# Kernel optimization log

Hardware: AMD Instinct MI355X
Metric: run time of the kernel (lower is better)

The kernel has to match this reference:

```python
import jax, jax.numpy as jnp
import numpy as np

B, T, D, H = 8, 512, 1024, 16
DH = D // H
MAX_LEN = 512  # max_pos_encoding


def rel_pos_encoding(seq_len, dim):
    # Relative sinusoidal PE, full (non-causal) context, no hidden state.
    # positions: max_len-1 ... 1, 0, -1 ... -(max_len-1)
    pos = jnp.concatenate([
        jnp.arange(MAX_LEN - 1, 0, -1, dtype=jnp.float32),
        jnp.arange(0, -MAX_LEN, -1, dtype=jnp.float32),
    ])  # (2*max_len-1,)
    inv_freq = jnp.power(10000.0, -2.0 * jnp.arange(dim // 2, dtype=jnp.float32) / dim)
    ang = pos[:, None] * inv_freq[None, :]  # (2M-1, D/2)
    pe = jnp.zeros((2 * MAX_LEN - 1, dim), dtype=jnp.float32)
    pe = pe.at[:, 0::2].set(jnp.sin(ang)).at[:, 1::2].set(jnp.cos(ang))
    # non-causal slice: [max_len - seq_len : max_len - 1 + seq_len] -> 2T-1 rows
    return pe[MAX_LEN - seq_len: MAX_LEN - 1 + seq_len]


def rel_to_abs(s):
    # full-context skewing (Bello et al.): s is (B, H, T1, T2) with T2 = 2*T1 - 1
    b, h, t1, t2 = s.shape
    s = jnp.pad(s, ((0, 0), (0, 0), (0, 0), (0, 1)))
    s = s.reshape(b, h, t1 * (t2 + 1))
    s = jnp.pad(s, ((0, 0), (0, 0), (0, t2 - t1)))
    s = s.reshape(b, h, t1 + 1, t2)
    return s[:, :, :t1, t1 - 1:]  # (B, H, T1, T1)


def setup_inputs() -> dict:
    key = jax.random.key(0)
    ks = jax.random.split(key, 9)
    sc = 1.0 / np.sqrt(D)
    return {
        "x": jax.random.normal(ks[0], (B, T, D), dtype=jnp.float32),
        "Wq": jax.random.normal(ks[1], (D, D), dtype=jnp.float32) * sc,
        "bq": jnp.zeros((D,), dtype=jnp.float32),
        "Wk": jax.random.normal(ks[2], (D, D), dtype=jnp.float32) * sc,
        "bk": jnp.zeros((D,), dtype=jnp.float32),
        "Wv": jax.random.normal(ks[3], (D, D), dtype=jnp.float32) * sc,
        "bv": jnp.zeros((D,), dtype=jnp.float32),
        "Wp": jax.random.normal(ks[4], (D, D), dtype=jnp.float32) * sc,
        "bp": jnp.zeros((D,), dtype=jnp.float32),
        "Wo": jax.random.normal(ks[5], (D, D), dtype=jnp.float32) * sc,
        "bo": jnp.zeros((D,), dtype=jnp.float32),
        "u": jax.random.normal(ks[6], (D,), dtype=jnp.float32) * 0.02,
        "v": jax.random.normal(ks[7], (D,), dtype=jnp.float32) * 0.02,
    }


def reference(x, Wq, bq, Wk, bk, Wv, bv, Wp, bp, Wo, bo, u, v):
    b, t, d = x.shape
    Q = x @ Wq.T + bq
    K = x @ Wk.T + bk
    V = x @ Wv.T + bv
    Qu = Q + u
    Qv = Q + v
    # relative positional embeddings, projected: (2T-1, D)
    E = rel_pos_encoding(t, d) @ Wp.T + bp
    # split heads
    Qu = Qu.reshape(b, t, H, DH).transpose(0, 2, 1, 3)  # (B,H,T,dh)
    Qv = Qv.reshape(b, t, H, DH).transpose(0, 2, 1, 3)
    Kh = K.reshape(b, t, H, DH).transpose(0, 2, 1, 3)
    Vh = V.reshape(b, t, H, DH).transpose(0, 2, 1, 3)
    Eh = E.reshape(2 * t - 1, H, DH)  # (R,H,dh)
    att_scores_K = jnp.einsum("bhqd,bhkd->bhqk", Qu, Kh)
    att_scores_E = rel_to_abs(jnp.einsum("bhqd,rhd->bhqr", Qv, Eh))
    att_scores = (att_scores_K + att_scores_E) / jnp.sqrt(jnp.float32(DH))
    att_w = jax.nn.softmax(att_scores, axis=-1)
    O = jnp.einsum("bhqk,bhkd->bhqd", att_w, Vh)
    O = O.transpose(0, 2, 1, 3).reshape(b, t, d)
    return O @ Wo.T + bo
```

## Files before the change

kernel.cpp:

```cpp
#include <hip/hip_runtime.h>
#include <hip/hip_bf16.h>
#include <cmath>

using short8  = __attribute__((ext_vector_type(8))) short;
using f32x4   = __attribute__((ext_vector_type(4))) float;
using uint4v  = __attribute__((ext_vector_type(4))) unsigned;

#define DEV static __device__ __forceinline__

DEV unsigned short f2bf(float f) {
  union { float f; unsigned u; } v; v.f = f;
  unsigned r = v.u + 0x7FFFu + ((v.u >> 16) & 1u);
  return (unsigned short)(r >> 16);
}
DEV float bf2f(unsigned short b) {
  union { unsigned u; float f; } v; v.u = ((unsigned)b) << 16;
  return v.f;
}

DEV void async_copy16(const void* g, void* l) {
  __builtin_amdgcn_global_load_lds(
      (const __attribute__((address_space(1))) void*)g,
      (__attribute__((address_space(3))) void*)l, 16, 0, 0);
}

#define DPPF(x, ctrl)                                                     \
  __builtin_bit_cast(float, __builtin_amdgcn_update_dpp(                  \
      __builtin_bit_cast(int, (x)), __builtin_bit_cast(int, (x)), (ctrl), \
      0xF, 0xF, false))

DEV float rowmax16(float t) {
  t = fmaxf(t, DPPF(t, 0x128));
  t = fmaxf(t, DPPF(t, 0x124));
  t = fmaxf(t, DPPF(t, 0x122));
  t = fmaxf(t, DPPF(t, 0x121));
  return t;
}
DEV float rowsum16(float t) {
  t += DPPF(t, 0x128);
  t += DPPF(t, 0x124);
  t += DPPF(t, 0x122);
  t += DPPF(t, 0x121);
  return t;
}
DEV unsigned dpp_xor8(unsigned x) {
  return (unsigned)__builtin_amdgcn_update_dpp((int)x, (int)x, 0x128, 0xF, 0xF, false);
}

__global__ __launch_bounds__(256) void prep_kernel(
    const float* __restrict__ x,  const float* __restrict__ Wq,
    const float* __restrict__ Wk, const float* __restrict__ Wv,
    const float* __restrict__ Wp, const float* __restrict__ Wo,
    const float* __restrict__ bq, const float* __restrict__ bk,
    const float* __restrict__ bv,
    unsigned short* __restrict__ xb, unsigned short* __restrict__ Wqkvb,
    unsigned short* __restrict__ Wpb, unsigned short* __restrict__ Wob,
    unsigned short* __restrict__ peb, float* __restrict__ bqkv) {
  const int blk = blockIdx.x;
  const int tid = threadIdx.x;
  if (blk < 9216) {
    const float* src;
    unsigned short* dst;
    int i;
    if (blk < 4096) {
      src = x; dst = xb; i = blk * 256 + tid;
    } else {
      const int w = (blk - 4096) >> 10;
      i = ((blk - 4096) & 1023) * 256 + tid;
      if      (w == 0) { src = Wq; dst = Wqkvb; }
      else if (w == 1) { src = Wk; dst = Wqkvb + 1048576; }
      else if (w == 2) { src = Wv; dst = Wqkvb + 2097152; }
      else if (w == 3) { src = Wp; dst = Wpb; }
      else             { src = Wo; dst = Wob; }
    }
    float4 v = ((const float4*)src)[i];
    ushort4 o;
    o.x = f2bf(v.x); o.y = f2bf(v.y); o.z = f2bf(v.z); o.w = f2bf(v.w);
    ((ushort4*)dst)[i] = o;
  } else if (blk < 11264) {
    const int idx = (blk - 9216) * 256 + tid;
    const int r = idx >> 9;
    const int m = idx & 511;
    const float inv_freq = __expf((float)m * -0.017988946039016004f);
    const float ang = (float)(511 - r) * inv_freq;
    peb[(size_t)r * 1024 + 2 * m]     = f2bf(sinf(ang));
    peb[(size_t)r * 1024 + 2 * m + 1] = f2bf(cosf(ang));
  } else {
    const int i = (blk - 11264) * 256 + tid;
    const float* s = (i < 1024) ? bq : (i < 2048) ? bk : bv;
    bqkv[i] = s[i & 1023];
  }
}

template <int OUTF32>
DEV void gemm_tile(const unsigned short* __restrict__ A,
                   const unsigned short* __restrict__ B,
                   const float* __restrict__ bias, void* __restrict__ Cout,
                   int N, int K, int m0, int n0, int tid,
                   unsigned short* sA, unsigned short* sB) {
  const int lane = tid & 63;
  const int wave = tid >> 6;

  const unsigned short* gA[4];
  const unsigned short* gB[4];
  unsigned ldst[4];
#pragma unroll
  for (int it = 0; it < 4; ++it) {
    unsigned o = (unsigned)(it * 4096 + wave * 1024 + lane * 16);
    unsigned row = o >> 7;
    unsigned x = (o & 127u) ^ ((row & 7u) << 4);
    ldst[it] = it * 4096 + wave * 1024;
    gA[it] = A + (size_t)(m0 + (int)row) * K + (x >> 1);
    gB[it] = B + (size_t)(n0 + (int)row) * K + (x >> 1);
  }

  f32x4 acc[4][4];
#pragma unroll
  for (int i = 0; i < 4; ++i)
#pragma unroll
    for (int j = 0; j < 4; ++j) acc[i][j] = f32x4{0.f, 0.f, 0.f, 0.f};

  const int wm = (wave >> 1) << 6;
  const int wn = (wave & 1) << 6;
  const int rsel = lane & 15;
  const int ksel = (lane >> 4) << 4;

  for (int k0 = 0; k0 < K; k0 += 64) {
#pragma unroll
    for (int it = 0; it < 4; ++it) {
      async_copy16(gA[it] + k0, (char*)sA + ldst[it]);
      async_copy16(gB[it] + k0, (char*)sB + ldst[it]);
    }
    __syncthreads();
#pragma unroll
    for (int kb = 0; kb < 2; ++kb) {
      const int kbyte = kb * 64 + ksel;
      short8 af[4], bf8[4];
#pragma unroll
      for (int i = 0; i < 4; ++i) {
        const int ra = wm + i * 16 + rsel;
        af[i] = *(const short8*)((const char*)sA + ra * 128 + (kbyte ^ ((ra & 7) << 4)));
        const int rb = wn + i * 16 + rsel;
        bf8[i] = *(const short8*)((const char*)sB + rb * 128 + (kbyte ^ ((rb & 7) << 4)));
      }
#pragma unroll
      for (int i = 0; i < 4; ++i)
#pragma unroll
        for (int j = 0; j < 4; ++j)
          acc[i][j] = __builtin_amdgcn_mfma_f32_16x16x32_bf16(af[i], bf8[j], acc[i][j], 0, 0, 0);
    }
    __syncthreads();
  }

#pragma unroll
  for (int i = 0; i < 4; ++i) {
    const int row0 = m0 + wm + i * 16 + ((lane >> 4) << 2);
#pragma unroll
    for (int j = 0; j < 4; ++j) {
      const int col = n0 + wn + j * 16 + rsel;
      const float bb = bias[col];
#pragma unroll
      for (int r = 0; r < 4; ++r) {
        const float val = acc[i][j][r] + bb;
        if (OUTF32)
          ((float*)Cout)[(size_t)(row0 + r) * N + col] = val;
        else
          ((unsigned short*)Cout)[(size_t)(row0 + r) * N + col] = f2bf(val);
      }
    }
  }
}

__global__ __launch_bounds__(256) void gemm_qkv_e_kernel(
    const unsigned short* __restrict__ xb, const unsigned short* __restrict__ Wqkvb,
    const float* __restrict__ bqkv, unsigned short* __restrict__ QKVb,
    const unsigned short* __restrict__ peb, const unsigned short* __restrict__ Wpb,
    const float* __restrict__ bp, unsigned short* __restrict__ Eb) {
  __shared__ unsigned short sA[128 * 64];
  __shared__ unsigned short sB[128 * 64];
  const int cpx = 104;
  const int bid = (blockIdx.x & 7) * cpx + (blockIdx.x >> 3);
  if (bid < 768) {
    const int mt = bid / 24, nt = bid - mt * 24;
    gemm_tile<0>(xb, Wqkvb, bqkv, QKVb, 3072, 1024, mt << 7, nt << 7,
                 threadIdx.x, sA, sB);
  } else {
    const int b2 = bid - 768;
    gemm_tile<0>(peb, Wpb, bp, Eb, 1024, 1024, (b2 >> 3) << 7, (b2 & 7) << 7,
                 threadIdx.x, sA, sB);
  }
}

__global__ __launch_bounds__(256) void gemm_out_kernel(
    const unsigned short* __restrict__ Ob, const unsigned short* __restrict__ Wob,
    const float* __restrict__ bo, float* __restrict__ out) {
  __shared__ unsigned short sA[128 * 64];
  __shared__ unsigned short sB[128 * 64];
  const int cpx = 32;
  const int bid = (blockIdx.x & 7) * cpx + (blockIdx.x >> 3);
  gemm_tile<1>(Ob, Wob, bo, out, 1024, 1024, (bid >> 3) << 7, (bid & 7) << 7,
               threadIdx.x, sA, sB);
}

__global__ __launch_bounds__(256, 2) void attn_kernel(
    const unsigned short* __restrict__ QKV,
    const unsigned short* __restrict__ E,
    const float* __restrict__ uvec, const float* __restrict__ vvec,
    unsigned short* __restrict__ O) {
  __shared__ unsigned short sK[2 * 4096];
  __shared__ unsigned short sE[4 * 4096];
  __shared__ unsigned short sVt[2 * 4096];
  __shared__ unsigned short sP[4][2048];

  const int tid = threadIdx.x;
  const int lane = tid & 63;
  const int wave = tid >> 6;
  const int cpx = gridDim.x >> 3;
  const int bid = (blockIdx.x & 7) * cpx + (blockIdx.x >> 3);
  const int qt = bid & 3;
  const int h = (bid >> 2) & 15;
  const int b = bid >> 6;
  const int q0 = qt << 7;

  const int rsel = lane & 15;
  const int g = lane >> 4;
  const int ilocb = g << 2;
  const int cb0 = 96 - 32 * wave;

  const unsigned short* Qb = QKV + (size_t)b * 512 * 3072 + h * 64;
  const unsigned short* Kb = Qb + 1024;
  const unsigned short* Vb = Qb + 2048;

  const float sc = 0.125f * 1.44269504088896f;

  short8 v8b[2];
#pragma unroll
  for (int it = 0; it < 2; ++it) {
    const int c = it * 256 + tid;
    v8b[it] = *(const short8*)(Vb + (size_t)(c >> 3) * 3072 + ((c & 7) << 3));
  }
#pragma unroll
  for (int it = 0; it < 2; ++it) {
    const unsigned o = (unsigned)(it * 4096 + wave * 1024 + lane * 16);
    const unsigned row = o >> 7;
    const unsigned x = (o & 127u) ^ ((row & 7u) << 4);
    async_copy16(Kb + (size_t)row * 3072 + (x >> 1),
                 (char*)sK + it * 4096 + wave * 1024);
  }
#pragma unroll
  for (int hh = 0; hh < 3; ++hh) {
    const int H = 6 - 2 * qt + hh;
#pragma unroll
    for (int it = 0; it < 2; ++it) {
      const unsigned o = (unsigned)(it * 4096 + wave * 1024 + lane * 16);
      const unsigned row = o >> 7;
      const unsigned x = (o & 127u) ^ ((row & 7u) << 4);
      async_copy16(E + (size_t)(H * 64 + (int)row) * 1024 + h * 64 + (x >> 1),
                   (char*)sE + (H & 3) * 8192 + it * 4096 + wave * 1024);
    }
  }

  short8 aU[2][2], aV[2][2];
#pragma unroll
  for (int f = 0; f < 2; ++f) {
    const int qrow = q0 + 32 * wave + 16 * f + rsel;
    const int dob = g * 8;
#pragma unroll
    for (int kb = 0; kb < 2; ++kb) {
      short8 q8 = *(const short8*)(Qb + (size_t)qrow * 3072 + kb * 32 + dob);
#pragma unroll
      for (int j = 0; j < 8; ++j) {
        const float qf = bf2f((unsigned short)q8[j]);
        aU[f][kb][j] = (short)f2bf((qf + uvec[h * 64 + kb * 32 + dob + j]) * sc);
        aV[f][kb][j] = (short)f2bf((qf + vvec[h * 64 + kb * 32 + dob + j]) * sc);
      }
    }
  }

#pragma unroll
  for (int it = 0; it < 2; ++it) {
    const int c = it * 256 + tid;
    const int trow = c >> 3;
    const int db = (c & 7) << 3;
    const int odd = trow & 1;
    const int kp = (trow & ~1) * 2;
    const uint4v dw = __builtin_bit_cast(uint4v, v8b[it]);
#pragma unroll
    for (int p = 0; p < 4; ++p) {
      const unsigned mine = dw[p];
      const unsigned other = dpp_xor8(mine);
      const unsigned res = odd ? ((mine & 0xffff0000u) | (other >> 16))
                               : ((other << 16) | (mine & 0xffffu));
      const int d = db + 2 * p + odd;
      *(unsigned*)((char*)sVt + d * 128 + (kp ^ (((d ^ (d >> 3)) & 7) << 4))) = res;
    }
  }
#pragma unroll
  for (int it = 0; it < 2; ++it) {
    const int c = it * 256 + tid;
    v8b[it] = *(const short8*)(Vb + (size_t)(64 + (c >> 3)) * 3072 + ((c & 7) << 3));
  }

  int srcLn[4];
  bool hiSel[4];
#pragma unroll
  for (int r = 0; r < 4; ++r) {
    const int offs = 15 - (ilocb + r) + rsel;
    srcLn[r] = (lane & 48) | (offs & 15);
    hiSel[r] = offs >= 16;
  }

  float mrun[2][4], lrun[2][4];
  f32x4 oacc[2][4];
#pragma unroll
  for (int f = 0; f < 2; ++f)
#pragma unroll
    for (int r = 0; r < 4; ++r) { mrun[f][r] = -INFINITY; lrun[f][r] = 0.f; }
#pragma unroll
  for (int f = 0; f < 2; ++f)
#pragma unroll
    for (int n = 0; n < 4; ++n) oacc[f][n] = f32x4{0.f, 0.f, 0.f, 0.f};

  for (int kt = 0; kt < 8; ++kt) {
    const int k0 = kt << 6;
    const int cur = kt & 1;
    const int H0 = 6 - 2 * qt + kt;

    __syncthreads();

    if (kt < 7) {
      const int kn = k0 + 64;
#pragma unroll
      for (int it = 0; it < 2; ++it) {
        const unsigned o = (unsigned)(it * 4096 + wave * 1024 + lane * 16);
        const unsigned row = o >> 7;
        const unsigned x = (o & 127u) ^ ((row & 7u) << 4);
        async_copy16(Kb + (size_t)(kn + (int)row) * 3072 + (x >> 1),
                     (char*)sK + (cur ^ 1) * 8192 + it * 4096 + wave * 1024);
      }
      {
        const int H = H0 + 3;
#pragma unroll
        for (int it = 0; it < 2; ++it) {
          const unsigned o = (unsigned)(it * 4096 + wave * 1024 + lane * 16);
          const unsigned row = o >> 7;
          const unsigned x = (o & 127u) ^ ((row & 7u) << 4);
          async_copy16(E + (size_t)(H * 64 + (int)row) * 1024 + h * 64 + (x >> 1),
                       (char*)sE + (H & 3) * 8192 + it * 4096 + wave * 1024);
        }
      }
#pragma unroll
      for (int it = 0; it < 2; ++it) {
        const int c = it * 256 + tid;
        const int trow = c >> 3;
        const int db = (c & 7) << 3;
        const int odd = trow & 1;
        const int kp = (trow & ~1) * 2;
        const uint4v dw = __builtin_bit_cast(uint4v, v8b[it]);
#pragma unroll
        for (int p = 0; p < 4; ++p) {
          const unsigned mine = dw[p];
          const unsigned other = dpp_xor8(mine);
          const unsigned res = odd ? ((mine & 0xffff0000u) | (other >> 16))
                                   : ((other << 16) | (mine & 0xffffu));
          const int d = db + 2 * p + odd;
          *(unsigned*)((char*)sVt + (cur ^ 1) * 8192 + d * 128 +
                       (kp ^ (((d ^ (d >> 3)) & 7) << 4))) = res;
        }
      }
    }

    f32x4 skacc[2][4], gacc[2][5];
#pragma unroll
    for (int f = 0; f < 2; ++f) {
#pragma unroll
      for (int nf = 0; nf < 4; ++nf) skacc[f][nf] = f32x4{0.f, 0.f, 0.f, 0.f};
#pragma unroll
      for (int cf = 0; cf < 5; ++cf) gacc[f][cf] = f32x4{0.f, 0.f, 0.f, 0.f};
    }

    __builtin_amdgcn_s_setprio(1);
#pragma unroll
    for (int kb = 0; kb < 2; ++kb) {
      const int kbyte = kb * 64 + g * 16;
      const char* sKc = (const char*)sK + cur * 8192;
      short8 ka, kbb;
      {
        const int r0 = rsel, r1 = 16 + rsel;
        ka  = *(const short8*)(sKc + r0 * 128 + (kbyte ^ ((r0 & 7) << 4)));
        kbb = *(const short8*)(sKc + r1 * 128 + (kbyte ^ ((r1 & 7) << 4)));
      }
      skacc[0][0] = __builtin_amdgcn_mfma_f32_16x16x32_bf16(aU[0][kb], ka,  skacc[0][0], 0, 0, 0);
      skacc[1][0] = __builtin_amdgcn_mfma_f32_16x16x32_bf16(aU[1][kb], ka,  skacc[1][0], 0, 0, 0);
      skacc[0][1] = __builtin_amdgcn_mfma_f32_16x16x32_bf16(aU[0][kb], kbb, skacc[0][1], 0, 0, 0);
      skacc[1][1] = __builtin_amdgcn_mfma_f32_16x16x32_bf16(aU[1][kb], kbb, skacc[1][1], 0, 0, 0);
      {
        const int r0 = 32 + rsel, r1 = 48 + rsel;
        ka  = *(const short8*)(sKc + r0 * 128 + (kbyte ^ ((r0 & 7) << 4)));
        kbb = *(const short8*)(sKc + r1 * 128 + (kbyte ^ ((r1 & 7) << 4)));
      }
      skacc[0][2] = __builtin_amdgcn_mfma_f32_16x16x32_bf16(aU[0][kb], ka,  skacc[0][2], 0, 0, 0);
      skacc[1][2] = __builtin_amdgcn_mfma_f32_16x16x32_bf16(aU[1][kb], ka,  skacc[1][2], 0, 0, 0);
      skacc[0][3] = __builtin_amdgcn_mfma_f32_16x16x32_bf16(aU[0][kb], kbb, skacc[0][3], 0, 0, 0);
      skacc[1][3] = __builtin_amdgcn_mfma_f32_16x16x32_bf16(aU[1][kb], kbb, skacc[1][3], 0, 0, 0);
    }
    __builtin_amdgcn_sched_barrier(0);

    if (kt < 6) {
#pragma unroll
      for (int it = 0; it < 2; ++it) {
        const int c = it * 256 + tid;
        v8b[it] = *(const short8*)(Vb + (size_t)(k0 + 128 + (c >> 3)) * 3072 +
                                   ((c & 7) << 3));
      }
    }

#pragma unroll
    for (int kb = 0; kb < 2; ++kb) {
      const int kbyte = kb * 64 + g * 16;
      short8 e0, e1, e2;
#define LDE(cfu)                                                              \
  ({                                                                          \
    const int rowbase = cb0 + 16 * (cfu);                                     \
    const int rb = rowbase + rsel;                                            \
    const int slot = (H0 + (rowbase >> 6)) & 3;                               \
    *(const short8*)((const char*)sE + slot * 8192 + (rb & 63) * 128 +        \
                     (kbyte ^ ((rb & 7) << 4)));                              \
  })
      e0 = LDE(0); e1 = LDE(1); e2 = LDE(2);
      gacc[1][0] = __builtin_amdgcn_mfma_f32_16x16x32_bf16(aV[1][kb], e0, gacc[1][0], 0, 0, 0);
      gacc[0][0] = __builtin_amdgcn_mfma_f32_16x16x32_bf16(aV[0][kb], e1, gacc[0][0], 0, 0, 0);
      gacc[1][1] = __builtin_amdgcn_mfma_f32_16x16x32_bf16(aV[1][kb], e1, gacc[1][1], 0, 0, 0);
      gacc[0][1] = __builtin_amdgcn_mfma_f32_16x16x32_bf16(aV[0][kb], e2, gacc[0][1], 0, 0, 0);
      gacc[1][2] = __builtin_amdgcn_mfma_f32_16x16x32_bf16(aV[1][kb], e2, gacc[1][2], 0, 0, 0);
      e0 = LDE(3); e1 = LDE(4); e2 = LDE(5);
      gacc[0][2] = __builtin_amdgcn_mfma_f32_16x16x32_bf16(aV[0][kb], e0, gacc[0][2], 0, 0, 0);
      gacc[1][3] = __builtin_amdgcn_mfma_f32_16x16x32_bf16(aV[1][kb], e0, gacc[1][3], 0, 0, 0);
      gacc[0][3] = __builtin_amdgcn_mfma_f32_16x16x32_bf16(aV[0][kb], e1, gacc[0][3], 0, 0, 0);
      gacc[1][4] = __builtin_amdgcn_mfma_f32_16x16x32_bf16(aV[1][kb], e1, gacc[1][4], 0, 0, 0);
      gacc[0][4] = __builtin_amdgcn_mfma_f32_16x16x32_bf16(aV[0][kb], e2, gacc[0][4], 0, 0, 0);
#undef LDE
    }
    __builtin_amdgcn_s_setprio(0);

#pragma unroll
    for (int f = 0; f < 2; ++f)
#pragma unroll
      for (int r = 0; r < 4; ++r) {
        float gsh[5];
#pragma unroll
        for (int cf = 0; cf < 5; ++cf)
          gsh[cf] = __shfl(gacc[f][cf][r], srcLn[r], 64);
#pragma unroll
        for (int nf = 0; nf < 4; ++nf)
          skacc[f][nf][r] += hiSel[r] ? gsh[nf + 1] : gsh[nf];
      }

    float scl[2][4];
#pragma unroll
    for (int f = 0; f < 2; ++f) {
      float rsum[4];
#pragma unroll
      for (int r = 0; r < 4; ++r) {
        float t = fmaxf(fmaxf(skacc[f][0][r], skacc[f][1][r]),
                        fmaxf(skacc[f][2][r], skacc[f][3][r]));
        t = rowmax16(t);
        const float mnew = fmaxf(mrun[f][r], t);
        scl[f][r] = __builtin_amdgcn_exp2f(mrun[f][r] - mnew);
        mrun[f][r] = mnew;
        rsum[r] = 0.f;
      }
#pragma unroll
      for (int nf = 0; nf < 4; ++nf)
#pragma unroll
        for (int r = 0; r < 4; ++r) {
          const float p = __builtin_amdgcn_exp2f(skacc[f][nf][r] - mrun[f][r]);
          rsum[r] += p;
          const int rloc = 16 * f + ilocb + r;
          const int jb = (nf * 16 + rsel) * 2;
          *(unsigned short*)((char*)sP[wave] + rloc * 128 +
                             (jb ^ ((rloc & 7) << 4))) = f2bf(p);
        }
#pragma unroll
      for (int r = 0; r < 4; ++r)
        lrun[f][r] = lrun[f][r] * scl[f][r] + rowsum16(rsum[r]);
#pragma unroll
      for (int nf = 0; nf < 4; ++nf)
#pragma unroll
        for (int r = 0; r < 4; ++r) oacc[f][nf][r] *= scl[f][r];
    }

    __builtin_amdgcn_s_setprio(1);
#pragma unroll
    for (int kb = 0; kb < 2; ++kb) {
      const int kbyte = kb * 64 + g * 16;
      short8 ap[2];
#pragma unroll
      for (int f = 0; f < 2; ++f) {
        const int pr = 16 * f + rsel;
        ap[f] = *(const short8*)((const char*)sP[wave] + pr * 128 +
                                 (kbyte ^ ((pr & 7) << 4)));
      }
#pragma unroll
      for (int nf = 0; nf < 4; ++nf) {
        const int rv = nf * 16 + rsel;
        short8 vb8 = *(const short8*)((const char*)sVt + cur * 8192 + rv * 128 +
                                      (kbyte ^ (((rv ^ (rv >> 3)) & 7) << 4)));
#pragma unroll
        for (int f = 0; f < 2; ++f)
          oacc[f][nf] = __builtin_amdgcn_mfma_f32_16x16x32_bf16(
              ap[f], vb8, oacc[f][nf], 0, 0, 0);
      }
    }
    __builtin_amdgcn_s_setprio(0);
  }

#pragma unroll
  for (int f = 0; f < 2; ++f)
#pragma unroll
    for (int nf = 0; nf < 4; ++nf)
#pragma unroll
      for (int r = 0; r < 4; ++r) {
        const int t = q0 + 32 * wave + 16 * f + ilocb + r;
        const int col = h * 64 + nf * 16 + rsel;
        O[(size_t)(b * 512 + t) * 1024 + col] = f2bf(oacc[f][nf][r] / lrun[f][r]);
      }
}

extern "C" void kernel_launch(void* const* d_in, const int* in_sizes, int n_in,
                              void* d_out, int out_size, void* d_ws, size_t ws_size,
                              hipStream_t stream) {
  const float* x  = (const float*)d_in[0];
  const float* Wq = (const float*)d_in[1];
  const float* bq = (const float*)d_in[2];
  const float* Wk = (const float*)d_in[3];
  const float* bk = (const float*)d_in[4];
  const float* Wv = (const float*)d_in[5];
  const float* bv = (const float*)d_in[6];
  const float* Wp = (const float*)d_in[7];
  const float* bp = (const float*)d_in[8];
  const float* Wo = (const float*)d_in[9];
  const float* bo = (const float*)d_in[10];
  const float* u  = (const float*)d_in[11];
  const float* v  = (const float*)d_in[12];
  float* out = (float*)d_out;

  char* ws = (char*)d_ws;
  const size_t MB = 1024 * 1024;
  unsigned short* xb    = (unsigned short*)(ws);
  unsigned short* Wqkvb = (unsigned short*)(ws + 8 * MB);
  unsigned short* Wpb   = (unsigned short*)(ws + 14 * MB);
  unsigned short* Wob   = (unsigned short*)(ws + 16 * MB);
  unsigned short* peb   = (unsigned short*)(ws + 18 * MB);
  unsigned short* QKVb  = (unsigned short*)(ws + 20 * MB);
  unsigned short* Eb    = (unsigned short*)(ws + 44 * MB);
  unsigned short* Ob    = (unsigned short*)(ws + 46 * MB);
  float* bqkv           = (float*)(ws + 54 * MB);

  prep_kernel<<<dim3(11276), dim3(256), 0, stream>>>(
      x, Wq, Wk, Wv, Wp, Wo, bq, bk, bv, xb, Wqkvb, Wpb, Wob, peb, bqkv);

  gemm_qkv_e_kernel<<<dim3(832), dim3(256), 0, stream>>>(
      xb, Wqkvb, bqkv, QKVb, peb, Wpb, bp, Eb);
  attn_kernel<<<dim3(512), dim3(256), 0, stream>>>(QKVb, Eb, u, v, Ob);
  gemm_out_kernel<<<dim3(256), dim3(256), 0, stream>>>(Ob, Wob, bo, out);
}
```

Before: 113.1 us.

## Double-buffer GEMM LDS tiles and vectorize epilogue stores via transposed MFMA

The shared GEMM tile routine now keeps two LDS buffers and prefetches the next K-slice asynchronously while computing on the current one, dropping one barrier per iteration. Wave priority is raised during the MFMA phase. MFMA operands are swapped so each lane holds four consecutive output columns, which allows float4/ushort4 stores and vector bias loads in the epilogue. The trade-off is double the LDS per block, which may reduce occupancy, and correctness now depends on the single barrier ordering buffer reuse.

Result: no change. 112.2 us, median of 3 (-0.8%).

```diff
diff --git a/kernel.cpp b/kernel.cpp
--- a/kernel.cpp
+++ b/kernel.cpp
@@ -123,15 +123,28 @@
   const int wm = (wave >> 1) << 6;
   const int wn = (wave & 1) << 6;
   const int rsel = lane & 15;
-  const int ksel = (lane >> 4) << 4;
-
+  const int g = lane >> 4;
+  const int ksel = g << 4;
+
+#pragma unroll
+  for (int it = 0; it < 4; ++it) {
+    async_copy16(gA[it], (char*)sA + ldst[it]);
+    async_copy16(gB[it], (char*)sB + ldst[it]);
+  }
+
+  int cur = 0;
   for (int k0 = 0; k0 < K; k0 += 64) {
-#pragma unroll
-    for (int it = 0; it < 4; ++it) {
-      async_copy16(gA[it] + k0, (char*)sA + ldst[it]);
-      async_copy16(gB[it] + k0, (char*)sB + ldst[it]);
-    }
     __syncthreads();
+    if (k0 + 64 < K) {
+#pragma unroll
+      for (int it = 0; it < 4; ++it) {
+        async_copy16(gA[it] + k0 + 64, (char*)sA + (cur ^ 1) * 16384 + ldst[it]);
+        async_copy16(gB[it] + k0 + 64, (char*)sB + (cur ^ 1) * 16384 + ldst[it]);
+      }
+    }
+    const char* sAc = (const char*)sA + cur * 16384;
+    const char* sBc = (const char*)sB + cur * 16384;
+    __builtin_amdgcn_s_setprio(1);
 #pragma unroll
     for (int kb = 0; kb < 2; ++kb) {
       const int kbyte = kb * 64 + ksel;
@@ -139,33 +152,41 @@
 #pragma unroll
       for (int i = 0; i < 4; ++i) {
         const int ra = wm + i * 16 + rsel;
-        af[i] = *(const short8*)((const char*)sA + ra * 128 + (kbyte ^ ((ra & 7) << 4)));
+        af[i] = *(const short8*)(sAc + ra * 128 + (kbyte ^ ((ra & 7) << 4)));
         const int rb = wn + i * 16 + rsel;
-        bf8[i] = *(const short8*)((const char*)sB + rb * 128 + (kbyte ^ ((rb & 7) << 4)));
+        bf8[i] = *(const short8*)(sBc + rb * 128 + (kbyte ^ ((rb & 7) << 4)));
       }
 #pragma unroll
       for (int i = 0; i < 4; ++i)
 #pragma unroll
         for (int j = 0; j < 4; ++j)
-          acc[i][j] = __builtin_amdgcn_mfma_f32_16x16x32_bf16(af[i], bf8[j], acc[i][j], 0, 0, 0);
-    }
-    __syncthreads();
+          acc[i][j] = __builtin_amdgcn_mfma_f32_16x16x32_bf16(bf8[j], af[i], acc[i][j], 0, 0, 0);
+    }
+    __builtin_amdgcn_s_setprio(0);
+    cur ^= 1;
   }
 
 #pragma unroll
   for (int i = 0; i < 4; ++i) {
-    const int row0 = m0 + wm + i * 16 + ((lane >> 4) << 2);
+    const int row = m0 + wm + i * 16 + rsel;
 #pragma unroll
     for (int j = 0; j < 4; ++j) {
-      const int col = n0 + wn + j * 16 + rsel;
-      const float bb = bias[col];
-#pragma unroll
-      for (int r = 0; r < 4; ++r) {
-        const float val = acc[i][j][r] + bb;
-        if (OUTF32)
-          ((float*)Cout)[(size_t)(row0 + r) * N + col] = val;
-        else
-          ((unsigned short*)Cout)[(size_t)(row0 + r) * N + col] = f2bf(val);
+      const int col0 = n0 + wn + j * 16 + 4 * g;
+      const float4 bb = *(const float4*)(bias + col0);
+      if (OUTF32) {
+        float4 o;
+        o.x = acc[i][j][0] + bb.x;
+        o.y = acc[i][j][1] + bb.y;
+        o.z = acc[i][j][2] + bb.z;
+        o.w = acc[i][j][3] + bb.w;
+        *(float4*)&((float*)Cout)[(size_t)row * N + col0] = o;
+      } else {
+        ushort4 o;
+        o.x = f2bf(acc[i][j][0] + bb.x);
+        o.y = f2bf(acc[i][j][1] + bb.y);
+        o.z = f2bf(acc[i][j][2] + bb.z);
+        o.w = f2bf(acc[i][j][3] + bb.w);
+        *(ushort4*)&((unsigned short*)Cout)[(size_t)row * N + col0] = o;
       }
     }
   }
@@ -176,8 +197,8 @@
     const float* __restrict__ bqkv, unsigned short* __restrict__ QKVb,
     const unsigned short* __restrict__ peb, const unsigned short* __restrict__ Wpb,
     const float* __restrict__ bp, unsigned short* __restrict__ Eb) {
-  __shared__ unsigned short sA[128 * 64];
-  __shared__ unsigned short sB[128 * 64];
+  __shared__ unsigned short sA[2 * 128 * 64];
+  __shared__ unsigned short sB[2 * 128 * 64];
   const int cpx = 104;
   const int bid = (blockIdx.x & 7) * cpx + (blockIdx.x >> 3);
   if (bid < 768) {
@@ -194,8 +215,8 @@
 __global__ __launch_bounds__(256) void gemm_out_kernel(
     const unsigned short* __restrict__ Ob, const unsigned short* __restrict__ Wob,
     const float* __restrict__ bo, float* __restrict__ out) {
-  __shared__ unsigned short sA[128 * 64];
-  __shared__ unsigned short sB[128 * 64];
+  __shared__ unsigned short sA[2 * 128 * 64];
+  __shared__ unsigned short sB[2 * 128 * 64];
   const int cpx = 32;
   const int bid = (blockIdx.x & 7) * cpx + (blockIdx.x >> 3);
   gemm_tile<1>(Ob, Wob, bo, out, 1024, 1024, (bid >> 3) << 7, (bid & 7) << 7,
```
